# Kernel tuning notes

Measured on AMD Instinct MI355X. Metric: run time of the kernel, lower is better.

The kernel has to match this reference:

```python
import jax, jax.numpy as jnp
import numpy as np

IN_F = 2
DIM_H = 64
DT = 0.02          # step_size
INTENSITY = 40.0   # Poisson rate multiplier
RATE = jnp.array([10.0, 1.0], dtype=jnp.float32)  # Gamma rates per feature


def _xavier(key, fan_in, fan_out):
    lim = float(np.sqrt(6.0 / (fan_in + fan_out)))
    return jax.random.uniform(key, (fan_in, fan_out), minval=-lim, maxval=lim, dtype=jnp.float32)


def setup_inputs() -> dict:
    key = jax.random.key(0)
    k0, k1, k2 = jax.random.split(key, 3)
    Nsim, steps = 100000, 200
    z0 = jax.random.normal(k0, (Nsim, IN_F), dtype=jnp.float32)
    W1 = _xavier(k1, IN_F, DIM_H)
    b1 = jnp.zeros((DIM_H,), dtype=jnp.float32)
    W2 = _xavier(k2, DIM_H, IN_F)
    b2 = jnp.zeros((IN_F,), dtype=jnp.float32)
    diffusion = jnp.float32(1.0)
    return {"z0": z0, "W1": W1, "b1": b1, "W2": W2, "b2": b2,
            "diffusion": diffusion, "Nsim": Nsim, "steps": steps}


def _drift(x, W1, b1, W2, b2):
    # MLP: Linear(2,64) -> tanh -> Linear(64,2)
    h = jnp.tanh(x @ W1 + b1)
    return h @ W2 + b2


def reference(z0, W1, b1, W2, b2, diffusion, Nsim, steps):
    sqrt_dt = jnp.float32(np.sqrt(DT))
    n = z0.shape[0]

    def step(state, key):
        kp, kn, kg = jax.random.split(key, 3)
        # Poisson(intensity*dt) jump counts, shape [N,1]
        pois = jax.random.poisson(kp, INTENSITY * DT, (n, 1)).astype(jnp.float32)
        a = jnp.broadcast_to(pois, (n, IN_F))  # Gamma concentration per feature
        # Gamma(conc=pois, rate=RATE); conc==0 -> sample is exactly 0
        g = jax.random.gamma(kg, jnp.maximum(a, 1.0), dtype=jnp.float32) / RATE
        jump = jnp.where(a > 0, g, 0.0)
        noise = jax.random.normal(kn, (n, IN_F), dtype=jnp.float32)
        new_state = (state
                     + _drift(state, W1, b1, W2, b2) * DT
                     + diffusion * sqrt_dt * noise
                     + jump)
        return new_state, new_state

    keys = jax.random.split(jax.random.key(42), steps)
    _, path = jax.lax.scan(step, z0, keys)            # [steps, N, F]
    path = jnp.concatenate([z0[None], path], axis=0)   # [steps+1, N, F]
    return jnp.transpose(path, (1, 0, 2))              # [N, steps+1, F]
```

## Files before the change

### kernel.cpp

```cpp
#include <hip/hip_runtime.h>
#include <cstdint>
#include <cmath>

#define DEVINL __device__ __forceinline__

struct U2 { uint32_t a, b; };
typedef float v2f __attribute__((ext_vector_type(2)));

DEVINL uint32_t rotl32(uint32_t x, uint32_t r){ return (x << r) | (x >> (32u - r)); }

DEVINL U2 tf(uint32_t k0, uint32_t k1, uint32_t x0, uint32_t x1){
  const uint32_t k2 = k0 ^ k1 ^ 0x1BD11BDAu;
  x0 += k0; x1 += k1;
#define TFR(r) { x0 += x1; x1 = rotl32(x1,(r)); x1 ^= x0; }
  TFR(13) TFR(15) TFR(26) TFR(6)  x0 += k1; x1 += k2 + 1u;
  TFR(17) TFR(29) TFR(16) TFR(24) x0 += k2; x1 += k0 + 2u;
  TFR(13) TFR(15) TFR(26) TFR(6)  x0 += k0; x1 += k1 + 3u;
  TFR(17) TFR(29) TFR(16) TFR(24) x0 += k1; x1 += k2 + 4u;
  TFR(13) TFR(15) TFR(26) TFR(6)  x0 += k2; x1 += k0 + 5u;
#undef TFR
  U2 r; r.a = x0; r.b = x1; return r;
}

DEVINL uint32_t pbits(uint32_t k0, uint32_t k1, uint32_t idx){
  U2 r = tf(k0, k1, 0u, idx);
  return r.a ^ r.b;
}

DEVINL float u01(uint32_t bits){
  return __uint_as_float((bits >> 9) | 0x3F800000u) - 1.0f;
}

DEVINL float xla_logf(float xin){
  float xf = fmaxf(__uint_as_float(0x00800000u), xin);
  uint32_t ib = __float_as_uint(xf);
  float e = (float)((int)(ib >> 23) - 126);
  float x = __uint_as_float((ib & 0x807fffffu) | 0x3f000000u);
  bool m = x < 0.707106781186547524f;
  float t = m ? x : 0.0f;
  x = __fsub_rn(x, 1.0f);
  if (m) e = __fsub_rn(e, 1.0f);
  x = __fadd_rn(x, t);
  float z = __fmul_rn(x, x);
  float y = 7.0376836292e-2f;
  y = fmaf(y, x, -1.1514610310e-1f);
  y = fmaf(y, x,  1.1676998740e-1f);
  y = fmaf(y, x, -1.2420140846e-1f);
  y = fmaf(y, x,  1.4249322787e-1f);
  y = fmaf(y, x, -1.6668057665e-1f);
  y = fmaf(y, x,  2.0000714765e-1f);
  y = fmaf(y, x, -2.4999993993e-1f);
  y = fmaf(y, x,  3.3333331174e-1f);
  y = __fmul_rn(y, x);
  y = __fmul_rn(y, z);
  y = fmaf(e, -2.12194440e-4f, y);
  y = fmaf(z, -0.5f, y);
  x = __fadd_rn(x, y);
  x = fmaf(e, 0.693359375f, x);
  if (xin == 0.0f) x = __uint_as_float(0xff800000u);
  return x;
}

DEVINL float xla_log1pf(float v){
  float av = fabsf(v);
  if (av < 1e-4f) return __fmul_rn(__fadd_rn(__fmul_rn(-0.5f, v), 1.0f), v);
  return xla_logf(__fadd_rn(v, 1.0f));
}

DEVINL float erfinv32(float x){
  float xx = __fmul_rn(x, x);
  float w = -xla_log1pf(-xx);
  float p;
  if (w < 5.0f){
    float ww = __fsub_rn(w, 2.5f);
    p = 2.81022636e-08f;
    p = __fadd_rn( 3.43273939e-07f, __fmul_rn(p, ww));
    p = __fadd_rn(-3.5233877e-06f,  __fmul_rn(p, ww));
    p = __fadd_rn(-4.39150654e-06f, __fmul_rn(p, ww));
    p = __fadd_rn( 0.00021858087f,  __fmul_rn(p, ww));
    p = __fadd_rn(-0.00125372503f,  __fmul_rn(p, ww));
    p = __fadd_rn(-0.00417768164f,  __fmul_rn(p, ww));
    p = __fadd_rn( 0.246640727f,    __fmul_rn(p, ww));
    p = __fadd_rn( 1.50140941f,     __fmul_rn(p, ww));
  } else {
    float ww = __fsub_rn(sqrtf(w), 3.0f);
    p = -0.000200214257f;
    p = __fadd_rn( 0.000100950558f, __fmul_rn(p, ww));
    p = __fadd_rn( 0.00134934322f,  __fmul_rn(p, ww));
    p = __fadd_rn(-0.00367342844f,  __fmul_rn(p, ww));
    p = __fadd_rn( 0.00573950773f,  __fmul_rn(p, ww));
    p = __fadd_rn(-0.0076224613f,   __fmul_rn(p, ww));
    p = __fadd_rn( 0.00943887047f,  __fmul_rn(p, ww));
    p = __fadd_rn( 1.00167406f,     __fmul_rn(p, ww));
    p = __fadd_rn( 2.83297682f,     __fmul_rn(p, ww));
  }
  return __fmul_rn(p, x);
}

#define SQRT2F (__uint_as_float(0x3FB504F3u))
#define NLOF   (__uint_as_float(0xBF7FFFFFu))
#define SQDTF  ((float)0.14142135623730951)

DEVINL float normal_from_bits(uint32_t bits){
  float ff = u01(bits);
  float u = __fadd_rn(__fmul_rn(ff, 2.0f), NLOF);
  u = fmaxf(NLOF, u);
  return __fmul_rn(SQRT2F, erfinv32(u));
}

DEVINL float fast_tanh(float x){
  float ax = fabsf(x);
  float e = __expf(-2.0f * ax);
  float r = (1.0f - e) * __builtin_amdgcn_rcpf(1.0f + e);
  return __builtin_copysignf(r, x);
}

DEVINL v2f f2fma(v2f a, v2f b, v2f c){ return __builtin_elementwise_fma(a, b, c); }

DEVINL float gamma_one(uint32_t gk0, uint32_t gk1, float alpha){
  const float d = __fsub_rn(alpha, (1.0f/3.0f));
  const float c = (1.0f/3.0f) / sqrtf(d);
  U2 K = tf(gk0, gk1, 0u, 0u);
  for (;;) {
    U2 xk = tf(K.a, K.b, 0u, 1u);
    U2 Uk = tf(K.a, K.b, 0u, 2u);
    float xx, v;
    for (;;) {
      U2 sub = tf(xk.a, xk.b, 0u, 1u);
      uint32_t nb = pbits(sub.a, sub.b, 0u);
      xx = normal_from_bits(nb);
      v = __fadd_rn(1.0f, __fmul_rn(xx, c));
      if (v > 0.0f) break;
      xk = tf(xk.a, xk.b, 0u, 0u);
    }
    float X = __fmul_rn(xx, xx);
    float V = __fmul_rn(__fmul_rn(v, v), v);
    float U = u01(pbits(Uk.a, Uk.b, 0u));
    float sq = __fsub_rn(1.0f, __fmul_rn(0.0331f, __fmul_rn(X, X)));
    if (U < sq) return __fmul_rn(d, V);
    float lnU = xla_logf(U);
    float lnV = xla_logf(V);
    float rhs = __fadd_rn(__fmul_rn(X, 0.5f),
                          __fmul_rn(d, __fadd_rn(__fsub_rn(1.0f, V), lnV)));
    if (lnU < rhs) return __fmul_rn(d, V);
    K = tf(K.a, K.b, 0u, 0u);
  }
}

#define NPK 24
#define WSTRIDE (4 + 2*NPK)
#define KEYOFF 8
#define JOFF   16384

__global__ void setup_kernel(uint32_t* __restrict__ ws, int steps){
  int t = blockIdx.x * blockDim.x + threadIdx.x;
  if (t >= steps) return;
  U2 kt = tf(0u, 42u, 0u, (uint32_t)t);
  U2 kp = tf(kt.a, kt.b, 0u, 0u);
  U2 kn = tf(kt.a, kt.b, 0u, 1u);
  U2 kg = tf(kt.a, kt.b, 0u, 2u);
  uint32_t* p = ws + KEYOFF + (size_t)t * WSTRIDE;
  p[0] = kn.a; p[1] = kn.b;
  p[2] = kg.a; p[3] = kg.b;
  uint32_t r0 = kp.a, r1 = kp.b;
  for (int i = 0; i < NPK; ++i) {
    U2 sub = tf(r0, r1, 0u, 1u);
    U2 rn  = tf(r0, r1, 0u, 0u);
    p[4 + 2*i] = sub.a; p[5 + 2*i] = sub.b;
    r0 = rn.a; r1 = rn.b;
  }
}

#define PEL 4
__global__ __launch_bounds__(64) void pois_kernel(
    uint32_t* __restrict__ ws, const float* __restrict__ diffp,
    int N, int steps, uint32_t POFF, uint32_t COFF)
{
  const int lane = threadIdx.x;
  const int t = blockIdx.y;
  const int base = blockIdx.x * (64 * PEL);
  const uint32_t* __restrict__ p = ws + KEYOFF + (size_t)t * WSTRIDE;
  const float coef = __fmul_rn(diffp[0], SQDTF);

  int poisv[PEL];
  #pragma unroll
  for (int j = 0; j < PEL; ++j) poisv[j] = -1;

  int cur = 0;
  int e = base + lane;
  float lp = 0.0f; int k = 0;
  bool done = (e >= N);

  #pragma unroll 1
  for (int guard = 0; guard < PEL * NPK + PEL + 1; ++guard) {
    if (!__any(!done)) break;
    if (!done) {
      if (!(lp > -0.8f)) {
        poisv[cur] = k - 1;
        cur++;
        lp = 0.0f; k = 0;
        int ne = base + cur * 64 + lane;
        if (cur >= PEL || ne >= N) done = true;
        else e = ne;
      }
    }
    if (!done) {
      uint32_t bits = pbits(p[4 + 2*k], p[5 + 2*k], (uint32_t)e);
      lp = __fadd_rn(lp, xla_logf(u01(bits)));
      k++;
      if (k >= NPK) lp = -1.0f;
    }
  }

  float* jarr = (float*)(ws + JOFF);
  uint8_t* pb = (uint8_t*)ws + (size_t)POFF * 4u + (size_t)t * (size_t)N;
  const uint32_t kn0 = p[0], kn1 = p[1];
  int mycnt = 0;
  #pragma unroll
  for (int j = 0; j < PEL; ++j) {
    int ej = base + j * 64 + lane;
    if (ej < N) {
      pb[ej] = (uint8_t)poisv[j];
      float nf0 = normal_from_bits(pbits(kn0, kn1, 2u*(uint32_t)ej));
      float nf1 = normal_from_bits(pbits(kn0, kn1, 2u*(uint32_t)ej + 1u));
      size_t jb = (size_t)t * (size_t)(2*N) + 2u * (uint32_t)ej;
      jarr[jb]     = __fmul_rn(coef, nf0);
      jarr[jb + 1] = __fmul_rn(coef, nf1);
      if (poisv[j] > 0) mycnt++;
    }
  }
  int c = mycnt;
  #pragma unroll
  for (int off = 32; off > 0; off >>= 1) c += __shfl_xor(c, off, 64);
  if (lane == 0)
    ws[COFF + (size_t)t * gridDim.x + blockIdx.x] = (uint32_t)c;
}

__global__ __launch_bounds__(256) void prefix_kernel(
    uint32_t* __restrict__ ws, uint32_t COFF, uint32_t BOFF, int NB)
{
  __shared__ uint32_t ssum[256];
  int i = threadIdx.x;
  int chunk = (NB + 255) >> 8;
  int lo = i * chunk, hi = lo + chunk; if (hi > NB) hi = NB;
  uint32_t s = 0;
  for (int j = lo; j < hi; ++j) s += ws[COFF + j];
  ssum[i] = s;
  __syncthreads();
  if (i == 0) {
    uint32_t run = 0;
    for (int k = 0; k < 256; ++k) { uint32_t c = ssum[k]; ssum[k] = run; run += c; }
    ws[0] = run;
  }
  __syncthreads();
  uint32_t base = ssum[i];
  for (int j = lo; j < hi; ++j) { ws[BOFF + j] = base; base += ws[COFF + j]; }
}

__global__ __launch_bounds__(256) void scatter_kernel(
    uint32_t* __restrict__ ws, int N, int steps,
    uint32_t POFF, uint32_t BOFF, uint32_t WOFF, uint32_t CAP)
{
  __shared__ uint32_t cnts[4];
  int e = blockIdx.x * 256 + threadIdx.x;
  int t = blockIdx.y;
  bool act = e < N;
  uint32_t pv = 0;
  if (act) pv = ((const uint8_t*)ws)[(size_t)POFF*4u + (size_t)t*(size_t)N + (size_t)e];
  uint64_t b = __ballot(pv > 0);
  int lane = threadIdx.x & 63, w = threadIdx.x >> 6;
  if (lane == 0) cnts[w] = (uint32_t)__popcll(b);
  __syncthreads();
  uint32_t bid = (uint32_t)blockIdx.y * gridDim.x + blockIdx.x;
  uint32_t wb = ws[BOFF + bid];
  for (int w2 = 0; w2 < w; ++w2) wb += cnts[w2];
  if (pv > 0) {
    uint32_t rank = (uint32_t)__popcll(b & ((1ull << lane) - 1ull));
    uint32_t idx = wb + rank;
    if (idx < CAP)
      ws[WOFF + idx] = ((uint32_t)t << 23) | ((uint32_t)e << 6) | pv;
  }
}

__global__ __launch_bounds__(256) void gamma_kernel(
    uint32_t* __restrict__ ws, int N, uint32_t WOFF, uint32_t CAP)
{
  uint32_t total = ws[0]; if (total > CAP) total = CAP;
  uint32_t j = blockIdx.x * 256u + threadIdx.x;
  if (j >= 2u * total) return;
  uint32_t ent = ws[WOFF + (j >> 1)];
  uint32_t t = ent >> 23, e = (ent >> 6) & 0x1FFFFu, pv = ent & 0x3Fu;
  const uint32_t* __restrict__ p = ws + KEYOFF + (size_t)t * WSTRIDE;
  uint32_t f = j & 1u;
  U2 gk = tf(p[2], p[3], 0u, 2u*e + f);
  float s = gamma_one(gk.a, gk.b, (float)pv);
  float jv = f ? s : (s / 10.0f);
  float* jarr = (float*)(ws + JOFF);
  float* slot = &jarr[(size_t)t * (size_t)(2*N) + (size_t)(2u*e + f)];
  *slot = __fadd_rn(*slot, jv);
}

__global__ __launch_bounds__(256) void jump_kernel(
    uint32_t* __restrict__ ws, const float* __restrict__ diffp, int N, int steps)
{
  int e = blockIdx.x * 256 + threadIdx.x;
  int t = blockIdx.y;
  if (e >= N) return;
  const uint32_t* __restrict__ p = ws + KEYOFF + (size_t)t * WSTRIDE;
  const uint32_t ue = (uint32_t)e;
  const float coef = __fmul_rn(diffp[0], SQDTF);
  float lp = 0.0f; int k = 0;
  #pragma unroll 1
  for (int i = 0; i < NPK; ++i) {
    if (!(lp > -0.8f)) break;
    k++;
    uint32_t bits = pbits(p[4 + 2*i], p[5 + 2*i], ue);
    lp = __fadd_rn(lp, xla_logf(u01(bits)));
  }
  int pois = k - 1;
  float nf0 = normal_from_bits(pbits(p[0], p[1], 2u*ue));
  float nf1 = normal_from_bits(pbits(p[0], p[1], 2u*ue + 1u));
  float j0 = __fmul_rn(coef, nf0), j1 = __fmul_rn(coef, nf1);
  if (pois > 0) {
    uint32_t kg0 = p[2], kg1 = p[3];
    float alpha = (float)pois;
    U2 gk0 = tf(kg0, kg1, 0u, 2u*ue);
    j0 = __fadd_rn(j0, gamma_one(gk0.a, gk0.b, alpha) / 10.0f);
    U2 gk1 = tf(kg0, kg1, 0u, 2u*ue + 1u);
    j1 = __fadd_rn(j1, gamma_one(gk1.a, gk1.b, alpha));
  }
  float* jarr = (float*)(ws + JOFF);
  size_t jbase = (size_t)t * (size_t)(2*N) + (size_t)(2*e);
  jarr[jbase] = j0; jarr[jbase + 1] = j1;
}

#define IBLK 256
__global__ __launch_bounds__(IBLK) void integrate_kernel(
    const float* __restrict__ z0, const float* __restrict__ W1,
    const float* __restrict__ b1, const float* __restrict__ W2,
    const float* __restrict__ b2, const float* __restrict__ diffp,
    const uint32_t* __restrict__ ws, float* __restrict__ out,
    int N, int steps)
{
  __shared__ float smem[322];
  for (int k = threadIdx.x; k < 322; k += IBLK) {
    float v;
    if (k < 128)      v = W1[k];
    else if (k < 192) v = b1[k - 128];
    else if (k < 320) v = W2[k - 192];
    else              v = b2[k - 320];
    smem[k] = v;
  }
  __syncthreads();
  const float* sW1 = smem;
  const float* sb1 = smem + 128;
  const float* sW2 = smem + 192;
  const float* sb2 = smem + 320;

  int tid = blockIdx.x * IBLK + threadIdx.x;
  if (tid >= 2 * N) return;
  const int e = tid >> 1;
  const int f = tid & 1;
  const uint32_t utid = (uint32_t)tid;

  float x = z0[tid];
  const size_t obase = (size_t)e * (size_t)(steps + 1) * 2u + (size_t)f;
  out[obase] = x;

  const float DTf  = 0.02f;
  const int   hbase = f << 5;
  const float* __restrict__ jarr = (const float*)(ws + JOFF);

  for (int t = 0; t < steps; ++t) {
    float S = jarr[(size_t)t * (size_t)(2*N) + utid];

    float xo = __shfl_xor(x, 1, 64);
    float xf0 = (f == 0) ? x : xo;
    float xf1 = (f == 0) ? xo : x;
    v2f xv0 = (v2f){xf0, xf0};
    v2f xv1 = (v2f){xf1, xf1};
    v2f acc = (v2f){0.0f, 0.0f};
    #pragma unroll
    for (int j = 0; j < 16; ++j) {
      int h = hbase + 2*j;
      v2f w1lo = *(const v2f*)&sW1[h];
      v2f w1hi = *(const v2f*)&sW1[64 + h];
      v2f b1v  = *(const v2f*)&sb1[h];
      v2f pre  = f2fma(xv0, w1lo, f2fma(xv1, w1hi, b1v));
      float hv0 = fast_tanh(pre.x);
      float hv1 = fast_tanh(pre.y);
      v2f w2a = *(const v2f*)&sW2[2*h];
      v2f w2b = *(const v2f*)&sW2[2*h + 2];
      acc = f2fma((v2f){hv0, hv0}, w2a, acc);
      acc = f2fma((v2f){hv1, hv1}, w2b, acc);
    }
    float q0 = acc.x + __shfl_xor(acc.x, 1, 64);
    float q1 = acc.y + __shfl_xor(acc.y, 1, 64);
    float dr = sb2[f] + ((f == 0) ? q0 : q1);

    x = __fadd_rn(__fadd_rn(x, __fmul_rn(dr, DTf)), S);
    out[obase + (size_t)(t + 1) * 2u] = x;
  }
}

__global__ __launch_bounds__(64) void sim_fallback_kernel(
    const float* __restrict__ z0, const float* __restrict__ W1,
    const float* __restrict__ b1, const float* __restrict__ W2,
    const float* __restrict__ b2, const float* __restrict__ diffp,
    const uint32_t* __restrict__ ws, float* __restrict__ out,
    int N, int steps)
{
  __shared__ float smem[322];
  for (int k = threadIdx.x; k < 322; k += 64) {
    float v;
    if (k < 128)      v = W1[k];
    else if (k < 192) v = b1[k - 128];
    else if (k < 320) v = W2[k - 192];
    else              v = b2[k - 320];
    smem[k] = v;
  }
  __syncthreads();
  const float* sW1 = smem;
  const float* sb1 = smem + 128;
  const float* sW2 = smem + 192;
  const float* sb2 = smem + 320;

  int tid = blockIdx.x * 64 + threadIdx.x;
  if (tid >= 2 * N) return;
  const int e = tid >> 1;
  const int f = tid & 1;
  const uint32_t ue   = (uint32_t)e;
  const uint32_t utid = (uint32_t)tid;

  float x = z0[tid];
  const size_t obase = (size_t)e * (size_t)(steps + 1) * 2u + (size_t)f;
  out[obase] = x;

  const float DTf  = 0.02f;
  const float coef = __fmul_rn(diffp[0], SQDTF);
  const int   hbase = f << 5;

  for (int t = 0; t < steps; ++t) {
    const uint32_t* __restrict__ p = ws + KEYOFF + (size_t)t * WSTRIDE;
    int pois;
    {
      float lp = 0.0f;
      pois = NPK - 1;
      #pragma unroll 1
      for (int m = 0; m < NPK/2; ++m) {
        int i0 = 2*m + f;
        uint32_t bits = pbits(p[4 + 2*i0], p[5 + 2*i0], ue);
        float lmine = xla_logf(u01(bits));
        float lother = __shfl_xor(lmine, 1, 64);
        float la = (f == 0) ? lmine : lother;
        float lb = (f == 0) ? lother : lmine;
        float s1 = __fadd_rn(lp, la);
        float s2 = __fadd_rn(s1, lb);
        if (!(s1 > -0.8f)) { pois = 2*m; break; }
        if (!(s2 > -0.8f)) { pois = 2*m + 1; break; }
        lp = s2;
      }
    }
    float nf = normal_from_bits(pbits(p[0], p[1], utid));
    float jump = 0.0f;
    if (pois > 0) {
      U2 gk = tf(p[2], p[3], 0u, utid);
      float s = gamma_one(gk.a, gk.b, (float)pois);
      jump = (f == 0) ? (s / 10.0f) : s;
    }
    float xo = __shfl_xor(x, 1, 64);
    float xf0 = (f == 0) ? x : xo;
    float xf1 = (f == 0) ? xo : x;
    float p0 = 0.0f, p1 = 0.0f;
    #pragma unroll
    for (int i = 0; i < 32; ++i) {
      int h = hbase + i;
      float hv = fast_tanh(fmaf(xf0, sW1[h], fmaf(xf1, sW1[64 + h], sb1[h])));
      p0 = fmaf(hv, sW2[2*h],     p0);
      p1 = fmaf(hv, sW2[2*h + 1], p1);
    }
    float q0 = p0 + __shfl_xor(p0, 1, 64);
    float q1 = p1 + __shfl_xor(p1, 1, 64);
    float dr = sb2[f] + ((f == 0) ? q0 : q1);
    x = __fadd_rn(__fadd_rn(__fadd_rn(x, __fmul_rn(dr, DTf)),
                            __fmul_rn(coef, nf)), jump);
    out[obase + (size_t)(t + 1) * 2u] = x;
  }
}

extern "C" void kernel_launch(void* const* d_in, const int* in_sizes, int n_in,
                              void* d_out, int out_size, void* d_ws, size_t ws_size,
                              hipStream_t stream) {
  const float* z0  = (const float*)d_in[0];
  const float* W1  = (const float*)d_in[1];
  const float* b1  = (const float*)d_in[2];
  const float* W2  = (const float*)d_in[3];
  const float* b2  = (const float*)d_in[4];
  const float* dif = (const float*)d_in[5];
  int N = in_sizes[0] / 2;
  int steps = out_size / (N * 2) - 1;
  uint32_t* ws = (uint32_t*)d_ws;
  int total = 2 * N;

  hipLaunchKernelGGL(setup_kernel, dim3((steps + 255) / 256), dim3(256), 0, stream,
                     ws, steps);

  size_t JSZ = (size_t)2 * (size_t)N * (size_t)steps;
  size_t PSZ = ((size_t)N * (size_t)steps + 3u) / 4u;
  int    NBX = (N + 255) / 256;
  size_t NB  = (size_t)NBX * (size_t)steps;
  size_t CAP = ((size_t)N * (size_t)steps * 11u) / 16u;
  size_t POFFs = (size_t)JOFF + JSZ;
  size_t COFFs = POFFs + PSZ;
  size_t BOFFs = COFFs + NB;
  size_t WOFFs = BOFFs + NB;
  size_t need0 = (WOFFs + CAP) * 4u;
  size_t need1 = ((size_t)JOFF + JSZ) * 4u;
  bool pk = (N < (1 << 17)) && (steps < (1 << 9)) && (steps <= 314) &&
            (WOFFs + CAP < 0xFFFFFFFFull);

  if (pk && ws_size >= need0) {
    hipLaunchKernelGGL(pois_kernel, dim3(NBX, steps), dim3(64), 0, stream,
                       ws, dif, N, steps, (uint32_t)POFFs, (uint32_t)COFFs);
    hipLaunchKernelGGL(prefix_kernel, dim3(1), dim3(256), 0, stream,
                       ws, (uint32_t)COFFs, (uint32_t)BOFFs, (int)NB);
    hipLaunchKernelGGL(scatter_kernel, dim3(NBX, steps), dim3(256), 0, stream,
                       ws, N, steps, (uint32_t)POFFs, (uint32_t)BOFFs,
                       (uint32_t)WOFFs, (uint32_t)CAP);
    size_t gth = 2u * CAP;
    hipLaunchKernelGGL(gamma_kernel, dim3((gth + 255) / 256), dim3(256), 0, stream,
                       ws, N, (uint32_t)WOFFs, (uint32_t)CAP);
    hipLaunchKernelGGL(integrate_kernel, dim3((total + IBLK - 1) / IBLK), dim3(IBLK),
                       0, stream, z0, W1, b1, W2, b2, dif, ws, (float*)d_out, N, steps);
  } else if (steps <= 314 && ws_size >= need1) {
    hipLaunchKernelGGL(jump_kernel, dim3((N + 255) / 256, steps), dim3(256), 0, stream,
                       ws, dif, N, steps);
    hipLaunchKernelGGL(integrate_kernel, dim3((total + IBLK - 1) / IBLK), dim3(IBLK),
                       0, stream, z0, W1, b1, W2, b2, dif, ws, (float*)d_out, N, steps);
  } else {
    hipLaunchKernelGGL(sim_fallback_kernel, dim3((total + 63) / 64), dim3(64), 0, stream,
                       z0, W1, b1, W2, b2, dif, ws, (float*)d_out, N, steps);
  }
}
```

Before: 1.594 ms.

## Split MLP hidden units across four lanes per path and pair gamma features per thread

The integrate kernel now assigns four lanes per path, each handling 16 of the 64 hidden units, instead of two lanes each owning one feature and 32 hidden units. This shortens the serial per-step tanh chain, at the cost of an extra shuffle reduction and twice as many threads. Both features are read and written as float2, and only one lane stores the output. The gamma kernel now samples both features of an entry in one thread and does a single float2 read-modify-write, halving the thread count and the entry loads.

Result: faster. 1.542 ms (-3.3%).

```diff
diff --git a/kernel.cpp b/kernel.cpp
--- a/kernel.cpp
+++ b/kernel.cpp
@@ -287,17 +287,22 @@
 {
   uint32_t total = ws[0]; if (total > CAP) total = CAP;
   uint32_t j = blockIdx.x * 256u + threadIdx.x;
-  if (j >= 2u * total) return;
-  uint32_t ent = ws[WOFF + (j >> 1)];
+  if (j >= total) return;
+  uint32_t ent = ws[WOFF + j];
   uint32_t t = ent >> 23, e = (ent >> 6) & 0x1FFFFu, pv = ent & 0x3Fu;
   const uint32_t* __restrict__ p = ws + KEYOFF + (size_t)t * WSTRIDE;
-  uint32_t f = j & 1u;
-  U2 gk = tf(p[2], p[3], 0u, 2u*e + f);
-  float s = gamma_one(gk.a, gk.b, (float)pv);
-  float jv = f ? s : (s / 10.0f);
+  uint32_t kg0 = p[2], kg1 = p[3];
+  float alpha = (float)pv;
+  U2 gka = tf(kg0, kg1, 0u, 2u*e);
+  float s0 = gamma_one(gka.a, gka.b, alpha) / 10.0f;
+  U2 gkb = tf(kg0, kg1, 0u, 2u*e + 1u);
+  float s1 = gamma_one(gkb.a, gkb.b, alpha);
   float* jarr = (float*)(ws + JOFF);
-  float* slot = &jarr[(size_t)t * (size_t)(2*N) + (size_t)(2u*e + f)];
-  *slot = __fadd_rn(*slot, jv);
+  float2* slot = (float2*)&jarr[(size_t)t * (size_t)(2*N) + (size_t)(2u*e)];
+  float2 v = *slot;
+  v.x = __fadd_rn(v.x, s0);
+  v.y = __fadd_rn(v.y, s1);
+  *slot = v;
 }
 
 __global__ __launch_bounds__(256) void jump_kernel(
@@ -358,30 +363,29 @@
   const float* sb2 = smem + 320;
 
   int tid = blockIdx.x * IBLK + threadIdx.x;
-  if (tid >= 2 * N) return;
-  const int e = tid >> 1;
-  const int f = tid & 1;
-  const uint32_t utid = (uint32_t)tid;
-
-  float x = z0[tid];
-  const size_t obase = (size_t)e * (size_t)(steps + 1) * 2u + (size_t)f;
-  out[obase] = x;
+  const int e = tid >> 2;
+  const int s = tid & 3;
+  if (e >= N) return;
+
+  float2 xv = *(const float2*)&z0[2*e];
+  float x0 = xv.x, x1 = xv.y;
+  const size_t orow = (size_t)(steps + 1) * 2u;
+  float* op = out + (size_t)e * orow;
+  if (s == 0) *(float2*)&op[0] = xv;
 
   const float DTf  = 0.02f;
-  const int   hbase = f << 5;
-  const float* __restrict__ jarr = (const float*)(ws + JOFF);
+  const int   hbase = s << 4;
+  const float2* __restrict__ jarr2 = (const float2*)(ws + JOFF);
+  const float b20 = sb2[0], b21 = sb2[1];
 
   for (int t = 0; t < steps; ++t) {
-    float S = jarr[(size_t)t * (size_t)(2*N) + utid];
-
-    float xo = __shfl_xor(x, 1, 64);
-    float xf0 = (f == 0) ? x : xo;
-    float xf1 = (f == 0) ? xo : x;
-    v2f xv0 = (v2f){xf0, xf0};
-    v2f xv1 = (v2f){xf1, xf1};
+    float2 S = jarr2[(size_t)t * (size_t)N + (size_t)e];
+
+    v2f xv0 = (v2f){x0, x0};
+    v2f xv1 = (v2f){x1, x1};
     v2f acc = (v2f){0.0f, 0.0f};
     #pragma unroll
-    for (int j = 0; j < 16; ++j) {
+    for (int j = 0; j < 8; ++j) {
       int h = hbase + 2*j;
       v2f w1lo = *(const v2f*)&sW1[h];
       v2f w1hi = *(const v2f*)&sW1[64 + h];
@@ -394,12 +398,20 @@
       acc = f2fma((v2f){hv0, hv0}, w2a, acc);
       acc = f2fma((v2f){hv1, hv1}, w2b, acc);
     }
-    float q0 = acc.x + __shfl_xor(acc.x, 1, 64);
-    float q1 = acc.y + __shfl_xor(acc.y, 1, 64);
-    float dr = sb2[f] + ((f == 0) ? q0 : q1);
-
-    x = __fadd_rn(__fadd_rn(x, __fmul_rn(dr, DTf)), S);
-    out[obase + (size_t)(t + 1) * 2u] = x;
+    float q0 = acc.x, q1 = acc.y;
+    q0 = q0 + __shfl_xor(q0, 1, 64);
+    q1 = q1 + __shfl_xor(q1, 1, 64);
+    q0 = q0 + __shfl_xor(q0, 2, 64);
+    q1 = q1 + __shfl_xor(q1, 2, 64);
+    float dr0 = b20 + q0;
+    float dr1 = b21 + q1;
+
+    x0 = __fadd_rn(__fadd_rn(x0, __fmul_rn(dr0, DTf)), S.x);
+    x1 = __fadd_rn(__fadd_rn(x1, __fmul_rn(dr1, DTf)), S.y);
+    if (s == 0) {
+      float2 o; o.x = x0; o.y = x1;
+      *(float2*)&op[(size_t)(t + 1) * 2u] = o;
+    }
   }
 }
 
@@ -519,6 +531,8 @@
   bool pk = (N < (1 << 17)) && (steps < (1 << 9)) && (steps <= 314) &&
             (WOFFs + CAP < 0xFFFFFFFFull);
 
+  int total4 = 4 * N;
+
   if (pk && ws_size >= need0) {
     hipLaunchKernelGGL(pois_kernel, dim3(NBX, steps), dim3(64), 0, stream,
                        ws, dif, N, steps, (uint32_t)POFFs, (uint32_t)COFFs);
@@ -527,15 +541,14 @@
     hipLaunchKernelGGL(scatter_kernel, dim3(NBX, steps), dim3(256), 0, stream,
                        ws, N, steps, (uint32_t)POFFs, (uint32_t)BOFFs,
                        (uint32_t)WOFFs, (uint32_t)CAP);
-    size_t gth = 2u * CAP;
-    hipLaunchKernelGGL(gamma_kernel, dim3((gth + 255) / 256), dim3(256), 0, stream,
+    hipLaunchKernelGGL(gamma_kernel, dim3((CAP + 255) / 256), dim3(256), 0, stream,
                        ws, N, (uint32_t)WOFFs, (uint32_t)CAP);
-    hipLaunchKernelGGL(integrate_kernel, dim3((total + IBLK - 1) / IBLK), dim3(IBLK),
+    hipLaunchKernelGGL(integrate_kernel, dim3((total4 + IBLK - 1) / IBLK), dim3(IBLK),
                        0, stream, z0, W1, b1, W2, b2, dif, ws, (float*)d_out, N, steps);
   } else if (steps <= 314 && ws_size >= need1) {
     hipLaunchKernelGGL(jump_kernel, dim3((N + 255) / 256, steps), dim3(256), 0, stream,
                        ws, dif, N, steps);
-    hipLaunchKernelGGL(integrate_kernel, dim3((total + IBLK - 1) / IBLK), dim3(IBLK),
+    hipLaunchKernelGGL(integrate_kernel, dim3((total4 + IBLK - 1) / IBLK), dim3(IBLK),
                        0, stream, z0, W1, b1, W2, b2, dif, ws, (float*)d_out, N, steps);
   } else {
     hipLaunchKernelGGL(sim_fallback_kernel, dim3((total + 63) / 64), dim3(64), 0, stream,
```
